# Optimization experiments

Measured on AMD Instinct MI355X. Metric: run time of the kernel, lower is better.

## Reference

```python
import jax, jax.numpy as jnp
import numpy as np
import math

D_MODEL = 1024
N_HEAD = 16
D_HEAD = D_MODEL // N_HEAD  # 64
D_KMAP = 128
B, L = 4, 4096


def setup_inputs() -> dict:
    key = jax.random.key(0)
    ks = jax.random.split(key, 10)
    s = 1.0 / math.sqrt(D_MODEL)
    inp = {
        "x": jax.random.normal(ks[0], (B, L, D_MODEL), dtype=jnp.float32),
        "proj_mat": jax.random.normal(ks[1], (D_HEAD, D_KMAP), dtype=jnp.float32),
        "Wq": jax.random.uniform(ks[2], (D_MODEL, D_MODEL), minval=-s, maxval=s),
        "bq": jax.random.uniform(ks[3], (D_MODEL,), minval=-s, maxval=s),
        "Wk": jax.random.uniform(ks[4], (D_MODEL, D_MODEL), minval=-s, maxval=s),
        "bk": jax.random.uniform(ks[5], (D_MODEL,), minval=-s, maxval=s),
        "Wv": jax.random.uniform(ks[6], (D_MODEL, D_MODEL), minval=-s, maxval=s),
        "bv": jax.random.uniform(ks[7], (D_MODEL,), minval=-s, maxval=s),
        "Wo": jax.random.uniform(ks[8], (D_MODEL, D_MODEL), minval=-s, maxval=s),
        "bo": jax.random.uniform(ks[9], (D_MODEL,), minval=-s, maxval=s),
    }
    return inp


def _fourier_kernel(x, proj_mat):
    # x: [B,L,H,d_head] -> [B,L,H,2*d_kmap]
    p = jnp.einsum("blhd,dm->blhm", x, proj_mat) / math.sqrt(D_HEAD)
    return jnp.concatenate([jnp.cos(p), jnp.sin(p)], axis=-1) / math.sqrt(D_KMAP)


def reference(x, proj_mat, Wq, bq, Wk, bk, Wv, bv, Wo, bo):
    Bv, Lv, _ = x.shape
    q = (x @ Wq.T + bq).reshape(Bv, Lv, N_HEAD, D_HEAD)
    k = (x @ Wk.T + bk).reshape(Bv, Lv, N_HEAD, D_HEAD)
    v = (x @ Wv.T + bv).reshape(Bv, Lv, N_HEAD, D_HEAD)
    q_prime = _fourier_kernel(q, proj_mat)  # [B,L,H,2M]
    k_prime = _fourier_kernel(k, proj_mat)  # [B,L,H,2M]
    kv = jnp.einsum("blhm,blhd->bhmd", k_prime, v)  # [B,H,2M,d_head]
    out = jnp.einsum("blhm,bhmd->blhd", q_prime, kv)  # [B,L,H,d_head]
    out = out.reshape(Bv, Lv, D_MODEL)
    return out @ Wo.T + bo
```

## Files before the change

kernel.cpp:

```cpp
#include <hip/hip_runtime.h>
#include <cstddef>
#include <cstdint>


typedef __attribute__((ext_vector_type(8))) short s8v;
typedef __attribute__((ext_vector_type(4))) short s4v;
typedef __attribute__((ext_vector_type(4))) float f32x4;

#define MFMA_BF16(a, b, c) __builtin_amdgcn_mfma_f32_16x16x32_bf16((a), (b), (c), 0, 0, 0)

#define P_SCALE 0.125f
#define F_SCALE 0.08838834764831845f

static __device__ __forceinline__ unsigned short f2bf(float f) {
  unsigned int u = __float_as_uint(f);
  u += 0x7fffu + ((u >> 16) & 1u);
  return (unsigned short)(u >> 16);
}

static __device__ __forceinline__ void gload_lds16(const void* g, void* l) {
  __builtin_amdgcn_global_load_lds(
      (const __attribute__((address_space(1))) unsigned int*)g,
      (__attribute__((address_space(3))) unsigned int*)l, 16, 0, 0);
}

__global__ void conv_bf16_kernel(const float* __restrict__ src, short* __restrict__ dst, int n) {
  int i4 = (blockIdx.x * 256 + threadIdx.x) * 4;
  if (i4 < n) {
    float4 f = *(const float4*)(src + i4);
    s4v v;
    v[0] = (short)f2bf(f.x); v[1] = (short)f2bf(f.y);
    v[2] = (short)f2bf(f.z); v[3] = (short)f2bf(f.w);
    *(s4v*)(dst + i4) = v;
  }
}

__global__ void projT_kernel(const float* __restrict__ proj, short* __restrict__ projT) {
  int t = threadIdx.x;
#pragma unroll
  for (int i = 0; i < 32; ++i) {
    int idx = t + i * 256;
    int d = idx >> 7, m = idx & 127;
    projT[m * 64 + d] = (short)f2bf(proj[idx]);
  }
}

__global__ void qkv_gemm_kernel(const short* __restrict__ xb,
                                const short* __restrict__ Wqkv,
                                const float* __restrict__ bq_, const float* __restrict__ bk_,
                                const float* __restrict__ bv_,
                                short* __restrict__ qb, short* __restrict__ kb,
                                short* __restrict__ vT) {
  __shared__ __align__(16) short smem[17408];
  short* Al = smem;
  short* Bl = smem + 8192;

  const int t = threadIdx.x;
  const int bm = blockIdx.x, bn = blockIdx.y;
  const int row0 = bm * 128, n0 = bn * 128;
  const int lane = t & 63, w = t >> 6;
  const int wm = w & 1, wn = w >> 1;
  const int l15 = lane & 15, lq = lane >> 4;
  const int sx = (l15 & 7) * 8;

  f32x4 acc[4][4];
#pragma unroll
  for (int i = 0; i < 4; ++i)
#pragma unroll
    for (int j = 0; j < 4; ++j) acc[i][j] = (f32x4){0.f, 0.f, 0.f, 0.f};

  for (int k0 = 0; k0 < 1024; k0 += 64) {
#pragma unroll
    for (int i = 0; i < 4; ++i) {
      int c = t + i * 256;
      int r = c >> 3, cl = c & 7;
      int cg = cl ^ (r & 7);
      gload_lds16(xb   + (size_t)(row0 + r) * 1024 + k0 + cg * 8, Al + c * 8);
      gload_lds16(Wqkv + (size_t)(n0 + r) * 1024 + k0 + cg * 8, Bl + c * 8);
    }
    __syncthreads();
#pragma unroll
    for (int ks = 0; ks < 2; ++ks) {
      const int kb8 = (ks * 4 + lq) * 8;
      s8v af[4], bfr[4];
#pragma unroll
      for (int i = 0; i < 4; ++i)
        af[i] = *(s8v*)&Al[(wm * 64 + i * 16 + l15) * 64 + (kb8 ^ sx)];
#pragma unroll
      for (int j = 0; j < 4; ++j)
        bfr[j] = *(s8v*)&Bl[(wn * 64 + j * 16 + l15) * 64 + (kb8 ^ sx)];
#pragma unroll
      for (int i = 0; i < 4; ++i)
#pragma unroll
        for (int j = 0; j < 4; ++j)
          acc[i][j] = MFMA_BF16(af[i], bfr[j], acc[i][j]);
    }
    __syncthreads();
  }

  const int region = bn >> 3;
  if (region < 2) {
    const float* bias = (region == 0) ? bq_ : bk_;
    short* IM = smem;
#pragma unroll
    for (int j = 0; j < 4; ++j) {
      int cl = wn * 64 + j * 16 + l15;
      float bsv = bias[(n0 & 1023) + cl];
#pragma unroll
      for (int i = 0; i < 4; ++i)
#pragma unroll
        for (int r = 0; r < 4; ++r)
          IM[(wm * 64 + i * 16 + lq * 4 + r) * 136 + cl] = (short)f2bf(acc[i][j][r] + bsv);
    }
    __syncthreads();
    short* dst = (region == 0) ? qb : kb;
#pragma unroll
    for (int i = 0; i < 8; ++i) {
      int c = t + i * 256;
      int r = c >> 4, cc = c & 15;
      *(s8v*)&dst[(size_t)(row0 + r) * 1024 + (n0 & 1023) + cc * 8] =
          *(s8v*)&IM[r * 136 + cc * 8];
    }
  } else {
    short* IM = smem;
#pragma unroll
    for (int j = 0; j < 4; ++j) {
      int cl = wn * 64 + j * 16 + l15;
      float bsv = bv_[(n0 - 2048) + cl];
#pragma unroll
      for (int i = 0; i < 4; ++i) {
        s4v pk;
#pragma unroll
        for (int r = 0; r < 4; ++r) pk[r] = (short)f2bf(acc[i][j][r] + bsv);
        *(s4v*)&IM[cl * 136 + wm * 64 + i * 16 + lq * 4] = pk;
      }
    }
    __syncthreads();
    const int b = row0 >> 12;
    const int l0 = (bm & 31) * 128;
#pragma unroll
    for (int i = 0; i < 8; ++i) {
      int c = t + i * 256;
      int ci = c >> 4, cc = c & 15;
      int cv = (bn - 16) * 128 + ci;
      int grow = (b * 16 + (cv >> 6)) * 64 + (cv & 63);
      *(s8v*)&vT[(size_t)grow * 4096 + l0 + cc * 8] = *(s8v*)&IM[ci * 136 + cc * 8];
    }
  }
}

__global__ void kv_accum_kernel(const short* __restrict__ kb, const short* __restrict__ vT,
                                const short* __restrict__ projT, float* __restrict__ kv) {
  __shared__ __align__(16) short smem[26624];
  short* kt = smem;
  short* vt = smem + 4096;
  short* kpT = smem + 8192;

  const int t = threadIdx.x;
  const int bid = blockIdx.x;
  const int chunk = bid & 7, h = (bid >> 3) & 15, b = bid >> 7;
  const int lane = t & 63, w = t >> 6;
  const int l15 = lane & 15, lq = lane >> 4;
  const int sx = (l15 & 7) * 8;

  s8v pf[8][2];
#pragma unroll
  for (int nt = 0; nt < 8; ++nt)
#pragma unroll
    for (int ks = 0; ks < 2; ++ks)
      pf[nt][ks] = *(const s8v*)(projT + (size_t)(nt * 16 + l15) * 64 + ks * 32 + lq * 8);

  f32x4 kvacc[4][4];
#pragma unroll
  for (int i = 0; i < 4; ++i)
#pragma unroll
    for (int j = 0; j < 4; ++j) kvacc[i][j] = (f32x4){0.f, 0.f, 0.f, 0.f};

  for (int s = 0; s < 8; ++s) {
    const int l0s = chunk * 512 + s * 64;
#pragma unroll
    for (int i = 0; i < 2; ++i) {
      int c = t + i * 256;
      int r = c >> 3, cl = c & 7;
      int cg = cl ^ (r & 7);
      gload_lds16(kb + (size_t)(b * 4096 + l0s + r) * 1024 + h * 64 + cg * 8, kt + c * 8);
      gload_lds16(vT + (size_t)((b * 16 + h) * 64 + r) * 4096 + l0s + cg * 8, vt + c * 8);
    }
    __syncthreads();

    f32x4 pacc[8];
#pragma unroll
    for (int nt = 0; nt < 8; ++nt) pacc[nt] = (f32x4){0.f, 0.f, 0.f, 0.f};
#pragma unroll
    for (int ks = 0; ks < 2; ++ks) {
      const int kb8 = (ks * 4 + lq) * 8;
      s8v af = *(s8v*)&kt[(w * 16 + l15) * 64 + (kb8 ^ sx)];
#pragma unroll
      for (int nt = 0; nt < 8; ++nt) pacc[nt] = MFMA_BF16(af, pf[nt][ks], pacc[nt]);
    }
#pragma unroll
    for (int nt = 0; nt < 8; ++nt) {
      s4v cp, sp;
#pragma unroll
      for (int r = 0; r < 4; ++r) {
        float p = pacc[nt][r] * P_SCALE;
        float sv, cv;
        __sincosf(p, &sv, &cv);
        cp[r] = (short)f2bf(cv * F_SCALE);
        sp[r] = (short)f2bf(sv * F_SCALE);
      }
      int m = nt * 16 + l15;
      int rbase = w * 16 + lq * 4;
      *(s4v*)&kpT[m * 72 + rbase] = cp;
      *(s4v*)&kpT[(m + 128) * 72 + rbase] = sp;
    }
    __syncthreads();

#pragma unroll
    for (int ks = 0; ks < 2; ++ks) {
      const int kb8 = (ks * 4 + lq) * 8;
      s8v af[4], bf4[4];
#pragma unroll
      for (int i = 0; i < 4; ++i)
        af[i] = *(s8v*)&kpT[(w * 64 + i * 16 + l15) * 72 + ks * 32 + lq * 8];
#pragma unroll
      for (int j = 0; j < 4; ++j)
        bf4[j] = *(s8v*)&vt[(j * 16 + l15) * 64 + (kb8 ^ sx)];
#pragma unroll
      for (int i = 0; i < 4; ++i)
#pragma unroll
        for (int j = 0; j < 4; ++j)
          kvacc[i][j] = MFMA_BF16(af[i], bf4[j], kvacc[i][j]);
    }
    __syncthreads();
  }

  float* kvb = kv + ((size_t)(b * 16 + h) << 14);
#pragma unroll
  for (int i = 0; i < 4; ++i)
#pragma unroll
    for (int j = 0; j < 4; ++j)
#pragma unroll
      for (int r = 0; r < 4; ++r) {
        int m = w * 64 + i * 16 + lq * 4 + r;
        int d = j * 16 + l15;
        atomicAdd(kvb + (size_t)m * 64 + d, kvacc[i][j][r]);
      }
}

__global__ void kvT_kernel(const float* __restrict__ kv, short* __restrict__ kvT) {
  __shared__ short im[16896];
  const int t = threadIdx.x;
  const int bh = blockIdx.x;
  const float* src = kv + ((size_t)bh << 14);
#pragma unroll
  for (int i = 0; i < 64; ++i) {
    int idx = t + i * 256;
    int m = idx >> 6, d = idx & 63;
    im[d * 264 + m] = (short)f2bf(src[idx]);
  }
  __syncthreads();
#pragma unroll
  for (int i = 0; i < 8; ++i) {
    int c = t + i * 256;
    int d = c >> 5, cc = c & 31;
    *(s8v*)&kvT[(size_t)(bh * 64 + d) * 256 + cc * 8] = *(s8v*)&im[d * 264 + cc * 8];
  }
}

__global__ void attn_kernel(const short* __restrict__ qb, const short* __restrict__ projT,
                            const short* __restrict__ kvT, short* __restrict__ attnb) {
  __shared__ __align__(16) short smem[20992];
  short* qt = smem;
  short* qA = smem + 4096;
  short* kvt = smem + 12800;

  const int t = threadIdx.x;
  const int rt = blockIdx.x, h = blockIdx.y;
  const int row0 = rt * 64;
  const int b = row0 >> 12;
  const int lane = t & 63, w = t >> 6;
  const int l15 = lane & 15, lq = lane >> 4;
  const int sx = (l15 & 7) * 8;

  s8v pf[8][2];
#pragma unroll
  for (int nt = 0; nt < 8; ++nt)
#pragma unroll
    for (int ks = 0; ks < 2; ++ks)
      pf[nt][ks] = *(const s8v*)(projT + (size_t)(nt * 16 + l15) * 64 + ks * 32 + lq * 8);

#pragma unroll
  for (int i = 0; i < 2; ++i) {
    int c = t + i * 256;
    int r = c >> 3, cl = c & 7;
    int cg = cl ^ (r & 7);
    gload_lds16(qb + (size_t)(row0 + r) * 1024 + h * 64 + cg * 8, qt + c * 8);
  }
  __syncthreads();

  f32x4 pacc[8];
#pragma unroll
  for (int nt = 0; nt < 8; ++nt) pacc[nt] = (f32x4){0.f, 0.f, 0.f, 0.f};
#pragma unroll
  for (int ks = 0; ks < 2; ++ks) {
    const int kb8 = (ks * 4 + lq) * 8;
    s8v af = *(s8v*)&qt[(w * 16 + l15) * 64 + (kb8 ^ sx)];
#pragma unroll
    for (int nt = 0; nt < 8; ++nt) pacc[nt] = MFMA_BF16(af, pf[nt][ks], pacc[nt]);
  }

  f32x4 aacc[4];
#pragma unroll
  for (int j = 0; j < 4; ++j) aacc[j] = (f32x4){0.f, 0.f, 0.f, 0.f};

#pragma unroll
  for (int half = 0; half < 2; ++half) {
#pragma unroll
    for (int nt = 0; nt < 8; ++nt)
#pragma unroll
      for (int r = 0; r < 4; ++r) {
        float p = pacc[nt][r] * P_SCALE;
        float fv = (half == 0) ? __cosf(p) : __sinf(p);
        qA[(w * 16 + lq * 4 + r) * 136 + nt * 16 + l15] = (short)f2bf(fv * F_SCALE);
      }
#pragma unroll
    for (int i = 0; i < 4; ++i) {
      int c = t + i * 256;
      int d = c >> 4, cl = c & 15;
      int cg = cl ^ (d & 15);
      gload_lds16(kvT + (size_t)((b * 16 + h) * 64 + d) * 256 + half * 128 + cg * 8,
                  kvt + c * 8);
    }
    __syncthreads();
#pragma unroll
    for (int ks = 0; ks < 4; ++ks) {
      s8v af = *(s8v*)&qA[(w * 16 + l15) * 136 + ks * 32 + lq * 8];
#pragma unroll
      for (int j = 0; j < 4; ++j) {
        int row = j * 16 + l15;
        s8v bf4 = *(s8v*)&kvt[row * 128 + (((ks * 4 + lq) ^ l15) * 8)];
        aacc[j] = MFMA_BF16(af, bf4, aacc[j]);
      }
    }
    __syncthreads();
  }

#pragma unroll
  for (int j = 0; j < 4; ++j)
#pragma unroll
    for (int r = 0; r < 4; ++r)
      smem[(w * 16 + lq * 4 + r) * 72 + j * 16 + l15] = (short)f2bf(aacc[j][r]);
  __syncthreads();
#pragma unroll
  for (int i = 0; i < 2; ++i) {
    int c = t + i * 256;
    int r = c >> 3, cc = c & 7;
    *(s8v*)&attnb[(size_t)(row0 + r) * 1024 + h * 64 + cc * 8] = *(s8v*)&smem[r * 72 + cc * 8];
  }
}

__global__ void out_gemm_kernel(const short* __restrict__ attnb, const short* __restrict__ Wob,
                                const float* __restrict__ bo_, float* __restrict__ out) {
  __shared__ __align__(16) short smem[16384];
  short* Al = smem;
  short* Bl = smem + 8192;

  const int t = threadIdx.x;
  const int bm = blockIdx.x, bn = blockIdx.y;
  const int row0 = bm * 128, n0 = bn * 128;
  const int lane = t & 63, w = t >> 6;
  const int wm = w & 1, wn = w >> 1;
  const int l15 = lane & 15, lq = lane >> 4;
  const int sx = (l15 & 7) * 8;

  f32x4 acc[4][4];
#pragma unroll
  for (int i = 0; i < 4; ++i)
#pragma unroll
    for (int j = 0; j < 4; ++j) acc[i][j] = (f32x4){0.f, 0.f, 0.f, 0.f};

  for (int k0 = 0; k0 < 1024; k0 += 64) {
#pragma unroll
    for (int i = 0; i < 4; ++i) {
      int c = t + i * 256;
      int r = c >> 3, cl = c & 7;
      int cg = cl ^ (r & 7);
      gload_lds16(attnb + (size_t)(row0 + r) * 1024 + k0 + cg * 8, Al + c * 8);
      gload_lds16(Wob   + (size_t)(n0 + r) * 1024 + k0 + cg * 8, Bl + c * 8);
    }
    __syncthreads();
#pragma unroll
    for (int ks = 0; ks < 2; ++ks) {
      const int kb8 = (ks * 4 + lq) * 8;
      s8v af[4], bfr[4];
#pragma unroll
      for (int i = 0; i < 4; ++i)
        af[i] = *(s8v*)&Al[(wm * 64 + i * 16 + l15) * 64 + (kb8 ^ sx)];
#pragma unroll
      for (int j = 0; j < 4; ++j)
        bfr[j] = *(s8v*)&Bl[(wn * 64 + j * 16 + l15) * 64 + (kb8 ^ sx)];
#pragma unroll
      for (int i = 0; i < 4; ++i)
#pragma unroll
        for (int j = 0; j < 4; ++j)
          acc[i][j] = MFMA_BF16(af[i], bfr[j], acc[i][j]);
    }
    __syncthreads();
  }

#pragma unroll
  for (int j = 0; j < 4; ++j) {
    int cl = wn * 64 + j * 16 + l15;
    float bsv = bo_[n0 + cl];
#pragma unroll
    for (int i = 0; i < 4; ++i)
#pragma unroll
      for (int r = 0; r < 4; ++r)
        out[(size_t)(row0 + wm * 64 + i * 16 + lq * 4 + r) * 1024 + n0 + cl] =
            acc[i][j][r] + bsv;
  }
}

extern "C" void kernel_launch(void* const* d_in, const int* in_sizes, int n_in,
                              void* d_out, int out_size, void* d_ws, size_t ws_size,
                              hipStream_t stream) {
  const float* x    = (const float*)d_in[0];
  const float* proj = (const float*)d_in[1];
  const float* Wq   = (const float*)d_in[2];
  const float* bq   = (const float*)d_in[3];
  const float* Wk   = (const float*)d_in[4];
  const float* bk   = (const float*)d_in[5];
  const float* Wv   = (const float*)d_in[6];
  const float* bv   = (const float*)d_in[7];
  const float* Wo   = (const float*)d_in[8];
  const float* bo   = (const float*)d_in[9];
  float* out = (float*)d_out;

  char* wsb = (char*)d_ws;
  short* qb    = (short*)(wsb + 0);
  short* kb    = (short*)(wsb + 33554432);
  short* vT    = (short*)(wsb + 67108864);
  short* xb    = (short*)(wsb + 100663296);
  short* Wqkvb = (short*)(wsb + 134217728);
  short* Wob   = (short*)(wsb + 140509184);
  short* projT = (short*)(wsb + 142606336);
  float* kv    = (float*)(wsb + 100663296);
  short* attnb = kb;
  short* kvT   = vT;

  const int WN = 1024 * 1024;
  conv_bf16_kernel<<<dim3(16384), dim3(256), 0, stream>>>(x, xb, 16777216);
  conv_bf16_kernel<<<dim3(WN / 1024), dim3(256), 0, stream>>>(Wq, Wqkvb, WN);
  conv_bf16_kernel<<<dim3(WN / 1024), dim3(256), 0, stream>>>(Wk, Wqkvb + WN, WN);
  conv_bf16_kernel<<<dim3(WN / 1024), dim3(256), 0, stream>>>(Wv, Wqkvb + 2 * WN, WN);
  conv_bf16_kernel<<<dim3(WN / 1024), dim3(256), 0, stream>>>(Wo, Wob, WN);
  projT_kernel<<<dim3(1), dim3(256), 0, stream>>>(proj, projT);

  qkv_gemm_kernel<<<dim3(128, 24), dim3(256), 0, stream>>>(x ? xb : xb, Wqkvb, bq, bk, bv, qb, kb, vT);
  hipMemsetAsync(kv, 0, 4194304, stream);
  kv_accum_kernel<<<dim3(512), dim3(256), 0, stream>>>(kb, vT, projT, kv);
  kvT_kernel<<<dim3(64), dim3(256), 0, stream>>>(kv, kvT);
  attn_kernel<<<dim3(256, 16), dim3(256), 0, stream>>>(qb, projT, kvT, attnb);
  out_gemm_kernel<<<dim3(128, 8), dim3(256), 0, stream>>>(attnb, Wob, bo, out);
}
```

Before: 433.1 us.

## Double-buffer K loads in kv_accum and replace atomics with partial-sum reduction

The kv accumulation kernel now double-buffers K tiles in LDS so the next tile's load overlaps compute. Each warp computes the projection and cos or sin for all 64 rows into its own LDS region, which removes two of the three barriers per step but duplicates the projection work across warp pairs. The float atomicAdd into kv and the memset that zeroed it are replaced by per-block partial buffers, summed in the reduce/transpose kernel. The V tile is waited on only with a per-thread vmcnt, with no barrier afterwards, so another warp's LDS-DMA data may not be visible when it is read; this is a cross-warp race risk.

```diff
diff --git a/kernel.cpp b/kernel.cpp
--- a/kernel.cpp
+++ b/kernel.cpp
@@ -150,11 +150,12 @@
 }
 
 __global__ void kv_accum_kernel(const short* __restrict__ kb, const short* __restrict__ vT,
-                                const short* __restrict__ projT, float* __restrict__ kv) {
-  __shared__ __align__(16) short smem[26624];
-  short* kt = smem;
-  short* vt = smem + 4096;
-  short* kpT = smem + 8192;
+                                const short* __restrict__ projT, float* __restrict__ parts) {
+  __shared__ __align__(16) short smem[28672];
+  short* const ktb0 = smem;
+  short* const ktb1 = smem + 4096;
+  short* const vt   = smem + 8192;
+  short* const kpT  = smem + 12288;
 
   const int t = threadIdx.x;
   const int bid = blockIdx.x;
@@ -162,13 +163,22 @@
   const int lane = t & 63, w = t >> 6;
   const int l15 = lane & 15, lq = lane >> 4;
   const int sx = (l15 & 7) * 8;
-
-  s8v pf[8][2];
-#pragma unroll
-  for (int nt = 0; nt < 8; ++nt)
+  const int g = w & 1;
+  const int trig = w >> 1;
+
+  const int c0 = t, c1 = t + 256;
+  const int r0 = c0 >> 3, cg0 = (c0 & 7) ^ (r0 & 7);
+  const int r1 = c1 >> 3, cg1 = (c1 & 7) ^ (r1 & 7);
+
+  const short* kbase = kb + (size_t)(b * 4096 + chunk * 512) * 1024 + h * 64;
+  const short* vbase = vT + ((size_t)((b * 16 + h) * 64)) * 4096 + chunk * 512;
+
+  s8v pf[4][2];
+#pragma unroll
+  for (int ntl = 0; ntl < 4; ++ntl)
 #pragma unroll
     for (int ks = 0; ks < 2; ++ks)
-      pf[nt][ks] = *(const s8v*)(projT + (size_t)(nt * 16 + l15) * 64 + ks * 32 + lq * 8);
+      pf[ntl][ks] = *(const s8v*)(projT + (size_t)((g * 4 + ntl) * 16 + l15) * 64 + ks * 32 + lq * 8);
 
   f32x4 kvacc[4][4];
 #pragma unroll
@@ -176,66 +186,78 @@
 #pragma unroll
     for (int j = 0; j < 4; ++j) kvacc[i][j] = (f32x4){0.f, 0.f, 0.f, 0.f};
 
+  gload_lds16(kbase + (size_t)r0 * 1024 + cg0 * 8, ktb0 + c0 * 8);
+  gload_lds16(kbase + (size_t)r1 * 1024 + cg1 * 8, ktb0 + c1 * 8);
+
   for (int s = 0; s < 8; ++s) {
-    const int l0s = chunk * 512 + s * 64;
-#pragma unroll
-    for (int i = 0; i < 2; ++i) {
-      int c = t + i * 256;
-      int r = c >> 3, cl = c & 7;
-      int cg = cl ^ (r & 7);
-      gload_lds16(kb + (size_t)(b * 4096 + l0s + r) * 1024 + h * 64 + cg * 8, kt + c * 8);
-      gload_lds16(vT + (size_t)((b * 16 + h) * 64 + r) * 4096 + l0s + cg * 8, vt + c * 8);
-    }
-    __syncthreads();
-
-    f32x4 pacc[8];
-#pragma unroll
-    for (int nt = 0; nt < 8; ++nt) pacc[nt] = (f32x4){0.f, 0.f, 0.f, 0.f};
+    __syncthreads();
+
+    gload_lds16(vbase + (size_t)r0 * 4096 + s * 64 + cg0 * 8, vt + c0 * 8);
+    gload_lds16(vbase + (size_t)r1 * 4096 + s * 64 + cg1 * 8, vt + c1 * 8);
+    const int sp = (s < 7) ? s + 1 : 7;
+    short* ktn = ((s + 1) & 1) ? ktb1 : ktb0;
+    gload_lds16(kbase + (size_t)(sp * 64 + r0) * 1024 + cg0 * 8, ktn + c0 * 8);
+    gload_lds16(kbase + (size_t)(sp * 64 + r1) * 1024 + cg1 * 8, ktn + c1 * 8);
+
+    const short* kt = (s & 1) ? ktb1 : ktb0;
+
+    f32x4 pacc[4][4];
+#pragma unroll
+    for (int rt = 0; rt < 4; ++rt)
+#pragma unroll
+      for (int ntl = 0; ntl < 4; ++ntl) pacc[rt][ntl] = (f32x4){0.f, 0.f, 0.f, 0.f};
 #pragma unroll
     for (int ks = 0; ks < 2; ++ks) {
       const int kb8 = (ks * 4 + lq) * 8;
-      s8v af = *(s8v*)&kt[(w * 16 + l15) * 64 + (kb8 ^ sx)];
-#pragma unroll
-      for (int nt = 0; nt < 8; ++nt) pacc[nt] = MFMA_BF16(af, pf[nt][ks], pacc[nt]);
-    }
-#pragma unroll
-    for (int nt = 0; nt < 8; ++nt) {
-      s4v cp, sp;
-#pragma unroll
-      for (int r = 0; r < 4; ++r) {
-        float p = pacc[nt][r] * P_SCALE;
-        float sv, cv;
-        __sincosf(p, &sv, &cv);
-        cp[r] = (short)f2bf(cv * F_SCALE);
-        sp[r] = (short)f2bf(sv * F_SCALE);
+      s8v af[4];
+#pragma unroll
+      for (int rt = 0; rt < 4; ++rt)
+        af[rt] = *(const s8v*)&kt[(rt * 16 + l15) * 64 + (kb8 ^ sx)];
+#pragma unroll
+      for (int rt = 0; rt < 4; ++rt)
+#pragma unroll
+        for (int ntl = 0; ntl < 4; ++ntl)
+          pacc[rt][ntl] = MFMA_BF16(af[rt], pf[ntl][ks], pacc[rt][ntl]);
+    }
+
+    short* kp = kpT + w * 4096;
+#pragma unroll
+    for (int rt = 0; rt < 4; ++rt)
+#pragma unroll
+      for (int ntl = 0; ntl < 4; ++ntl) {
+        s4v pk;
+#pragma unroll
+        for (int r = 0; r < 4; ++r) {
+          float p = pacc[rt][ntl][r] * P_SCALE;
+          float fv = trig ? __sinf(p) : __cosf(p);
+          pk[r] = (short)f2bf(fv * F_SCALE);
+        }
+        int m = ntl * 16 + l15;
+        int rowc = rt * 2 + (lq >> 1);
+        *(s4v*)&kp[m * 64 + (((rowc ^ (m & 7)) << 3) | ((lq & 1) << 2))] = pk;
       }
-      int m = nt * 16 + l15;
-      int rbase = w * 16 + lq * 4;
-      *(s4v*)&kpT[m * 72 + rbase] = cp;
-      *(s4v*)&kpT[(m + 128) * 72 + rbase] = sp;
-    }
-    __syncthreads();
+
+    asm volatile("s_waitcnt vmcnt(2)" ::: "memory");
 
 #pragma unroll
     for (int ks = 0; ks < 2; ++ks) {
       const int kb8 = (ks * 4 + lq) * 8;
-      s8v af[4], bf4[4];
-#pragma unroll
-      for (int i = 0; i < 4; ++i)
-        af[i] = *(s8v*)&kpT[(w * 64 + i * 16 + l15) * 72 + ks * 32 + lq * 8];
+      s8v akv[4], bkv[4];
+#pragma unroll
+      for (int i = 0; i < 4; ++i)
+        akv[i] = *(const s8v*)&kp[(i * 16 + l15) * 64 + (kb8 ^ sx)];
 #pragma unroll
       for (int j = 0; j < 4; ++j)
-        bf4[j] = *(s8v*)&vt[(j * 16 + l15) * 64 + (kb8 ^ sx)];
+        bkv[j] = *(const s8v*)&vt[(j * 16 + l15) * 64 + (kb8 ^ sx)];
 #pragma unroll
       for (int i = 0; i < 4; ++i)
 #pragma unroll
         for (int j = 0; j < 4; ++j)
-          kvacc[i][j] = MFMA_BF16(af[i], bf4[j], kvacc[i][j]);
-    }
-    __syncthreads();
-  }
-
-  float* kvb = kv + ((size_t)(b * 16 + h) << 14);
+          kvacc[i][j] = MFMA_BF16(akv[i], bkv[j], kvacc[i][j]);
+    }
+  }
+
+  float* pb = parts + ((size_t)bid << 14);
 #pragma unroll
   for (int i = 0; i < 4; ++i)
 #pragma unroll
@@ -244,20 +266,22 @@
       for (int r = 0; r < 4; ++r) {
         int m = w * 64 + i * 16 + lq * 4 + r;
         int d = j * 16 + l15;
-        atomicAdd(kvb + (size_t)m * 64 + d, kvacc[i][j][r]);
+        pb[(size_t)m * 64 + d] = kvacc[i][j][r];
       }
 }
 
-__global__ void kvT_kernel(const float* __restrict__ kv, short* __restrict__ kvT) {
+__global__ void kv_reduce_kernel(const float* __restrict__ parts, short* __restrict__ kvT) {
   __shared__ short im[16896];
   const int t = threadIdx.x;
   const int bh = blockIdx.x;
-  const float* src = kv + ((size_t)bh << 14);
-#pragma unroll
+  const float* p0 = parts + ((size_t)bh << 17);
+#pragma unroll 4
   for (int i = 0; i < 64; ++i) {
     int idx = t + i * 256;
-    int m = idx >> 6, d = idx & 63;
-    im[d * 264 + m] = (short)f2bf(src[idx]);
+    float s = 0.f;
+#pragma unroll
+    for (int c = 0; c < 8; ++c) s += p0[(c << 14) + idx];
+    im[(idx & 63) * 264 + (idx >> 6)] = (short)f2bf(s);
   }
   __syncthreads();
 #pragma unroll
@@ -445,7 +469,7 @@
   short* Wqkvb = (short*)(wsb + 134217728);
   short* Wob   = (short*)(wsb + 140509184);
   short* projT = (short*)(wsb + 142606336);
-  float* kv    = (float*)(wsb + 100663296);
+  float* parts = (float*)(wsb + 100663296);
   short* attnb = kb;
   short* kvT   = vT;
 
@@ -457,10 +481,9 @@
   conv_bf16_kernel<<<dim3(WN / 1024), dim3(256), 0, stream>>>(Wo, Wob, WN);
   projT_kernel<<<dim3(1), dim3(256), 0, stream>>>(proj, projT);
 
-  qkv_gemm_kernel<<<dim3(128, 24), dim3(256), 0, stream>>>(x ? xb : xb, Wqkvb, bq, bk, bv, qb, kb, vT);
-  hipMemsetAsync(kv, 0, 4194304, stream);
-  kv_accum_kernel<<<dim3(512), dim3(256), 0, stream>>>(kb, vT, projT, kv);
-  kvT_kernel<<<dim3(64), dim3(256), 0, stream>>>(kv, kvT);
+  qkv_gemm_kernel<<<dim3(128, 24), dim3(256), 0, stream>>>(xb, Wqkvb, bq, bk, bv, qb, kb, vT);
+  kv_accum_kernel<<<dim3(512), dim3(256), 0, stream>>>(kb, vT, projT, parts);
+  kv_reduce_kernel<<<dim3(64), dim3(256), 0, stream>>>(parts, kvT);
   attn_kernel<<<dim3(256, 16), dim3(256), 0, stream>>>(qb, projT, kvT, attnb);
   out_gemm_kernel<<<dim3(128, 8), dim3(256), 0, stream>>>(attnb, Wob, bo, out);
 }
```

New measurement: 508.4 us. 1.17x slower.
